# Kernel tuning notes

Hardware: AMD Instinct MI355X
Metric: run time of the kernel (lower is better)

Reference implementation:

```python
import jax, jax.numpy as jnp
import numpy as np

BN_EPS = 1e-5


def setup_inputs() -> dict:
    key = jax.random.key(0)
    ks = jax.random.split(key, 6)
    B, Adim, Bdim, E, An, Bn = 16, 512, 512, 256, 2048, 2048
    return {
        "input_A": jax.random.normal(ks[0], (B, Adim, An), jnp.float32),
        "input_B": jax.random.normal(ks[1], (B, Bdim, Bn), jnp.float32),
        "W_A": jax.random.normal(ks[2], (E, Adim), jnp.float32) * (1.0 / np.sqrt(Adim)),
        "W_B": jax.random.normal(ks[3], (E, Bdim), jnp.float32) * (1.0 / np.sqrt(Bdim)),
        "W_Bh": jax.random.normal(ks[4], (E, Bdim), jnp.float32) * (1.0 / np.sqrt(Bdim)),
        "W_out": jax.random.normal(ks[5], (Bdim, E), jnp.float32) * (1.0 / np.sqrt(E)),
        "bn_gamma": jnp.ones((Bdim,), jnp.float32),
        "bn_beta": jnp.zeros((Bdim,), jnp.float32),
    }


def reference(input_A, input_B, W_A, W_B, W_Bh, W_out, bn_gamma, bn_beta):
    # 1x1 conv == per-position linear projection over channel dim
    A = jnp.einsum("ec,bcn->ben", W_A, input_A)    # [B, E, A_n]
    Bp = jnp.einsum("ec,bcn->ben", W_B, input_B)    # [B, E, B_n]
    Bh = jnp.einsum("ec,bcn->ben", W_Bh, input_B)   # [B, E, B_n]

    norm = jnp.sqrt(jnp.float32(A.shape[1]))
    h = jnp.einsum("bea,bem->bam", A, Bp) / norm    # [B, A_n, B_n]
    att = jax.nn.softmax(h, axis=2)                 # softmax over B_n

    out = jnp.einsum("bem,bam->bea", Bh, att)       # bmm(B_h, att^T): [B, E, A_n]
    out = jnp.einsum("ce,bea->bca", W_out, out)     # [B, Bdim, A_n]

    # BatchNorm1d (training mode): per-channel stats over (batch, positions)
    mean = jnp.mean(out, axis=(0, 2), keepdims=True)
    var = jnp.mean(jnp.square(out - mean), axis=(0, 2), keepdims=True)
    out = (out - mean) * jax.lax.rsqrt(var + BN_EPS)
    out = out * bn_gamma[None, :, None] + bn_beta[None, :, None]
    return out, att
```

## Files before the change

kernel.cpp:

```cpp
#include <hip/hip_runtime.h>
#include <cstdint>
#include <cstddef>

#define BATCH 16
#define CDIM 512
#define EDIM 256
#define NDIM 2048

typedef short bf16x8 __attribute__((ext_vector_type(8)));
typedef float f32x4 __attribute__((ext_vector_type(4)));

__device__ __forceinline__ unsigned short f2bf(float f) {
  union { float f; unsigned int u; } v; v.f = f;
  unsigned int r = v.u + 0x7fffu + ((v.u >> 16) & 1u);
  return (unsigned short)(r >> 16);
}

__global__ __launch_bounds__(256) void cast_f32_bf16(const float* __restrict__ x,
                                                     unsigned short* __restrict__ y) {
  const int i = (blockIdx.x * 256 + threadIdx.x) * 4;
  float4 v = *(const float4*)&x[i];
  ushort4 o;
  o.x = f2bf(v.x); o.y = f2bf(v.y); o.z = f2bf(v.z); o.w = f2bf(v.w);
  *(ushort4*)&y[i] = o;
}

__global__ __launch_bounds__(256) void transpose_cast(const float* __restrict__ X,
                                                      unsigned short* __restrict__ Xt) {
  __shared__ float tile[32][33];
  const int b = blockIdx.z;
  const float* Xb = X + (size_t)b * CDIM * NDIM;
  unsigned short* Xtb = Xt + (size_t)b * CDIM * NDIM;
  const int n0 = blockIdx.x * 32, c0 = blockIdx.y * 32;
  const int tx = threadIdx.x & 31, ty = threadIdx.x >> 5;
#pragma unroll
  for (int i = 0; i < 4; ++i)
    tile[ty + i * 8][tx] = Xb[(size_t)(c0 + ty + i * 8) * NDIM + n0 + tx];
  __syncthreads();
  const int nl = threadIdx.x >> 3, c4 = (threadIdx.x & 7) * 4;
  ushort4 o;
  o.x = f2bf(tile[c4 + 0][nl]); o.y = f2bf(tile[c4 + 1][nl]);
  o.z = f2bf(tile[c4 + 2][nl]); o.w = f2bf(tile[c4 + 3][nl]);
  *(ushort4*)&Xtb[(size_t)(n0 + nl) * CDIM + c0 + c4] = o;
}

enum { OUT_F32 = 0, OUT_BF16 = 1, OUT_BF16T = 2 };

template <int OUTMODE, bool B_IS_F32>
__global__ __launch_bounds__(256) void gemm_nt_mfma(
    const void* __restrict__ Ap, const void* __restrict__ Bptr, void* __restrict__ Cp,
    int M, int N, int K, long sA, long sB, long sC, float scale) {
  __shared__ alignas(16) short As[128 * 72];
  __shared__ alignas(16) short Bs[128 * 72];
  const int b = blockIdx.z;
  const int m0 = blockIdx.y * 128, n0 = blockIdx.x * 128;
  const unsigned short* A = (const unsigned short*)Ap + (size_t)sA * b;
  const int tid = threadIdx.x;
  const int lane = tid & 63, wid = tid >> 6;
  const int l16 = lane & 15, q = lane >> 4;
  const int wm = (wid >> 1) * 64, wn = (wid & 1) * 64;
  const int sr = tid >> 1, sh = tid & 1;

  f32x4 acc[4][4];
#pragma unroll
  for (int i = 0; i < 4; ++i)
#pragma unroll
    for (int j = 0; j < 4; ++j) acc[i][j] = f32x4{0.f, 0.f, 0.f, 0.f};

  short* a_dst = &As[sr * 72 + sh * 32];
  short* b_dst = &Bs[sr * 72 + sh * 32];

  for (int k0 = 0; k0 < K; k0 += 64) {
    {
      const unsigned short* src = A + (size_t)(m0 + sr) * K + k0 + sh * 32;
      int4 c0 = *(const int4*)(src);
      int4 c1 = *(const int4*)(src + 8);
      int4 c2 = *(const int4*)(src + 16);
      int4 c3 = *(const int4*)(src + 24);
      *(int4*)(a_dst) = c0;
      *(int4*)(a_dst + 8) = c1;
      *(int4*)(a_dst + 16) = c2;
      *(int4*)(a_dst + 24) = c3;
    }
    if (B_IS_F32) {
      const float* src = (const float*)Bptr + (size_t)sB * b + (size_t)(n0 + sr) * K + k0 + sh * 32;
#pragma unroll
      for (int c = 0; c < 8; ++c) {
        float4 v = *(const float4*)(src + c * 4);
        ushort4 o;
        o.x = f2bf(v.x); o.y = f2bf(v.y); o.z = f2bf(v.z); o.w = f2bf(v.w);
        *(ushort4*)(b_dst + c * 4) = o;
      }
    } else {
      const unsigned short* src =
          (const unsigned short*)Bptr + (size_t)sB * b + (size_t)(n0 + sr) * K + k0 + sh * 32;
      int4 c0 = *(const int4*)(src);
      int4 c1 = *(const int4*)(src + 8);
      int4 c2 = *(const int4*)(src + 16);
      int4 c3 = *(const int4*)(src + 24);
      *(int4*)(b_dst) = c0;
      *(int4*)(b_dst + 8) = c1;
      *(int4*)(b_dst + 16) = c2;
      *(int4*)(b_dst + 24) = c3;
    }
    __syncthreads();
#pragma unroll
    for (int kk = 0; kk < 2; ++kk) {
      bf16x8 af[4], bfr[4];
#pragma unroll
      for (int t = 0; t < 4; ++t)
        af[t] = *(const bf16x8*)&As[(wm + t * 16 + l16) * 72 + kk * 32 + q * 8];
#pragma unroll
      for (int t = 0; t < 4; ++t)
        bfr[t] = *(const bf16x8*)&Bs[(wn + t * 16 + l16) * 72 + kk * 32 + q * 8];
#pragma unroll
      for (int i = 0; i < 4; ++i)
#pragma unroll
        for (int j = 0; j < 4; ++j)
          acc[i][j] = __builtin_amdgcn_mfma_f32_16x16x32_bf16(af[i], bfr[j], acc[i][j], 0, 0, 0);
    }
    __syncthreads();
  }

  const int mb = m0 + wm + q * 4, nb = n0 + wn + l16;
  if (OUTMODE == OUT_F32) {
    float* C = (float*)Cp + (size_t)sC * b;
#pragma unroll
    for (int i = 0; i < 4; ++i)
#pragma unroll
      for (int j = 0; j < 4; ++j)
#pragma unroll
        for (int r = 0; r < 4; ++r)
          C[(size_t)(mb + i * 16 + r) * N + nb + j * 16] = acc[i][j][r] * scale;
  } else if (OUTMODE == OUT_BF16) {
    unsigned short* C = (unsigned short*)Cp + (size_t)sC * b;
#pragma unroll
    for (int i = 0; i < 4; ++i)
#pragma unroll
      for (int j = 0; j < 4; ++j)
#pragma unroll
        for (int r = 0; r < 4; ++r)
          C[(size_t)(mb + i * 16 + r) * N + nb + j * 16] = f2bf(acc[i][j][r]);
  } else {
    unsigned short* C = (unsigned short*)Cp + (size_t)sC * b;
#pragma unroll
    for (int i = 0; i < 4; ++i)
#pragma unroll
      for (int j = 0; j < 4; ++j) {
        ushort4 o;
        o.x = f2bf(acc[i][j][0]); o.y = f2bf(acc[i][j][1]);
        o.z = f2bf(acc[i][j][2]); o.w = f2bf(acc[i][j][3]);
        *(ushort4*)&C[(size_t)(nb + j * 16) * M + mb + i * 16] = o;
      }
  }
}

__global__ __launch_bounds__(256) void softmax_rows(float* __restrict__ att) {
  float4* p = (float4*)(att + (size_t)blockIdx.x * NDIM);
  const int tid = threadIdx.x;
  float4 v0 = p[tid];
  float4 v1 = p[tid + 256];

  float m = fmaxf(fmaxf(fmaxf(v0.x, v0.y), fmaxf(v0.z, v0.w)),
                  fmaxf(fmaxf(v1.x, v1.y), fmaxf(v1.z, v1.w)));
#pragma unroll
  for (int off = 32; off; off >>= 1) m = fmaxf(m, __shfl_down(m, off));
  __shared__ float redm[4];
  if ((tid & 63) == 0) redm[tid >> 6] = m;
  __syncthreads();
  m = fmaxf(fmaxf(redm[0], redm[1]), fmaxf(redm[2], redm[3]));

  v0.x = __expf(v0.x - m); v0.y = __expf(v0.y - m);
  v0.z = __expf(v0.z - m); v0.w = __expf(v0.w - m);
  v1.x = __expf(v1.x - m); v1.y = __expf(v1.y - m);
  v1.z = __expf(v1.z - m); v1.w = __expf(v1.w - m);

  float s = v0.x + v0.y + v0.z + v0.w + v1.x + v1.y + v1.z + v1.w;
#pragma unroll
  for (int off = 32; off; off >>= 1) s += __shfl_down(s, off);
  __shared__ float reds[4];
  if ((tid & 63) == 0) reds[tid >> 6] = s;
  __syncthreads();
  s = reds[0] + reds[1] + reds[2] + reds[3];

  const float inv = 1.0f / s;
  v0.x *= inv; v0.y *= inv; v0.z *= inv; v0.w *= inv;
  v1.x *= inv; v1.y *= inv; v1.z *= inv; v1.w *= inv;
  p[tid] = v0;
  p[tid + 256] = v1;
}

__global__ __launch_bounds__(256) void bn_stats(const float* __restrict__ o,
                                                float* __restrict__ mean,
                                                float* __restrict__ rstd) {
  const int c = blockIdx.x;
  const int tid = threadIdx.x;
  float s = 0.f, sq = 0.f;
  for (int b = 0; b < BATCH; ++b) {
    const float4* p = (const float4*)(o + ((size_t)b * CDIM + c) * NDIM);
    float4 v = p[tid];
    float4 w = p[tid + 256];
    s += v.x + v.y + v.z + v.w + w.x + w.y + w.z + w.w;
    sq += v.x * v.x + v.y * v.y + v.z * v.z + v.w * v.w +
          w.x * w.x + w.y * w.y + w.z * w.z + w.w * w.w;
  }
#pragma unroll
  for (int off = 32; off; off >>= 1) {
    s += __shfl_down(s, off);
    sq += __shfl_down(sq, off);
  }
  __shared__ float rs[4], rq[4];
  if ((tid & 63) == 0) { rs[tid >> 6] = s; rq[tid >> 6] = sq; }
  __syncthreads();
  if (tid == 0) {
    s = rs[0] + rs[1] + rs[2] + rs[3];
    sq = rq[0] + rq[1] + rq[2] + rq[3];
    const float invn = 1.0f / (BATCH * NDIM);
    float mu = s * invn;
    float var = sq * invn - mu * mu;
    mean[c] = mu;
    rstd[c] = rsqrtf(var + 1e-5f);
  }
}

__global__ __launch_bounds__(256) void bn_norm(float* __restrict__ o,
                                               const float* __restrict__ mean,
                                               const float* __restrict__ rstd,
                                               const float* __restrict__ gamma,
                                               const float* __restrict__ beta) {
  const size_t i = (size_t)blockIdx.x * 256 + threadIdx.x;
  const int c = (int)((i >> 9) & (CDIM - 1));
  float4 v = ((float4*)o)[i];
  const float a = rstd[c] * gamma[c];
  const float d = beta[c] - mean[c] * a;
  v.x = v.x * a + d; v.y = v.y * a + d;
  v.z = v.z * a + d; v.w = v.w * a + d;
  ((float4*)o)[i] = v;
}

extern "C" void kernel_launch(void* const* d_in, const int* in_sizes, int n_in,
                              void* d_out, int out_size, void* d_ws, size_t ws_size,
                              hipStream_t stream) {
  const float* input_A = (const float*)d_in[0];
  const float* input_B = (const float*)d_in[1];
  const float* W_A   = (const float*)d_in[2];
  const float* W_B   = (const float*)d_in[3];
  const float* W_Bh  = (const float*)d_in[4];
  const float* W_out = (const float*)d_in[5];
  const float* gamma = (const float*)d_in[6];
  const float* beta  = (const float*)d_in[7];

  float* out = (float*)d_out;
  float* att = out + (size_t)BATCH * CDIM * NDIM;

  char* w = (char*)d_ws;
  unsigned short* wA  = (unsigned short*)(w + 0);
  unsigned short* wB  = (unsigned short*)(w + 262144);
  unsigned short* wBh = (unsigned short*)(w + 524288);
  unsigned short* wO  = (unsigned short*)(w + 786432);
  float* mean = (float*)(w + 1048576);
  float* rstd = (float*)(w + 1050624);
  char* base = w + 1056768;
  unsigned short* X_At = (unsigned short*)(base);
  unsigned short* X_Bt = (unsigned short*)(base + 33554432);
  unsigned short* A_t  = (unsigned short*)(base + 67108864);
  unsigned short* Bp_t = (unsigned short*)(base);
  unsigned short* Bh   = (unsigned short*)(base + 16777216);
  unsigned short* oute = (unsigned short*)(base + 67108864);

  const dim3 blk(256);

  cast_f32_bf16<<<dim3(128), blk, 0, stream>>>(W_A, wA);
  cast_f32_bf16<<<dim3(128), blk, 0, stream>>>(W_B, wB);
  cast_f32_bf16<<<dim3(128), blk, 0, stream>>>(W_Bh, wBh);
  cast_f32_bf16<<<dim3(128), blk, 0, stream>>>(W_out, wO);

  transpose_cast<<<dim3(64, 16, BATCH), blk, 0, stream>>>(input_A, X_At);
  transpose_cast<<<dim3(64, 16, BATCH), blk, 0, stream>>>(input_B, X_Bt);

  gemm_nt_mfma<OUT_BF16, false><<<dim3(2, 16, BATCH), blk, 0, stream>>>(
      X_At, wA, A_t, 2048, 256, 512, 1048576, 0, 524288, 1.f);
  gemm_nt_mfma<OUT_BF16, false><<<dim3(2, 16, BATCH), blk, 0, stream>>>(
      X_Bt, wB, Bp_t, 2048, 256, 512, 1048576, 0, 524288, 1.f);
  gemm_nt_mfma<OUT_BF16, false><<<dim3(16, 2, BATCH), blk, 0, stream>>>(
      wBh, X_Bt, Bh, 256, 2048, 512, 0, 1048576, 524288, 1.f);
  gemm_nt_mfma<OUT_F32, false><<<dim3(16, 16, BATCH), blk, 0, stream>>>(
      A_t, Bp_t, att, 2048, 2048, 256, 524288, 524288, 4194304, 0.0625f);

  softmax_rows<<<dim3(BATCH * NDIM), blk, 0, stream>>>(att);

  gemm_nt_mfma<OUT_BF16T, true><<<dim3(16, 2, BATCH), blk, 0, stream>>>(
      Bh, att, oute, 256, 2048, 2048, 524288, 4194304, 524288, 1.f);

  gemm_nt_mfma<OUT_F32, false><<<dim3(16, 4, BATCH), blk, 0, stream>>>(
      wO, oute, out, 512, 2048, 256, 0, 524288, 1048576, 1.f);

  bn_stats<<<dim3(CDIM), blk, 0, stream>>>(out, mean, rstd);
  bn_norm<<<dim3(16384), blk, 0, stream>>>(out, mean, rstd, gamma, beta);
}
```

Baseline: 768.3 us.

## Fuse attention score GEMM with row softmax in one kernel

Replaces the separate QK-style GEMM that wrote fp32 scores plus the row softmax kernel with one kernel. Each block computes a 16-row strip across all 2048 columns, keeping the scores in registers while double-buffering B tiles in LDS. It then does the max, exp and sum reductions and writes the normalized probabilities once. This removes one full write and read of the 256MB fp32 score tensor. In exchange each block does only small 16-row MFMA tiles, holds 128 accumulator registers, and stores with a strided pattern.

```diff
diff --git a/kernel.cpp b/kernel.cpp
--- a/kernel.cpp
+++ b/kernel.cpp
@@ -155,39 +155,125 @@
   }
 }
 
-__global__ __launch_bounds__(256) void softmax_rows(float* __restrict__ att) {
-  float4* p = (float4*)(att + (size_t)blockIdx.x * NDIM);
+#define BPAD 264
+
+__global__ __launch_bounds__(256, 2) void g3_softmax(
+    const unsigned short* __restrict__ At, const unsigned short* __restrict__ Bt,
+    float* __restrict__ att) {
+  __shared__ alignas(16) short As[16 * BPAD];
+  __shared__ alignas(16) short Bs[2][64 * BPAD];
+  __shared__ float redm[4][16];
+  __shared__ float reds[4][16];
+
+  const int b = blockIdx.y;
+  const int a0 = blockIdx.x * 16;
+  const unsigned short* Ab = At + (size_t)b * (NDIM * EDIM) + (size_t)a0 * EDIM;
+  const unsigned short* Bb = Bt + (size_t)b * (NDIM * EDIM);
   const int tid = threadIdx.x;
-  float4 v0 = p[tid];
-  float4 v1 = p[tid + 256];
-
-  float m = fmaxf(fmaxf(fmaxf(v0.x, v0.y), fmaxf(v0.z, v0.w)),
-                  fmaxf(fmaxf(v1.x, v1.y), fmaxf(v1.z, v1.w)));
-#pragma unroll
-  for (int off = 32; off; off >>= 1) m = fmaxf(m, __shfl_down(m, off));
-  __shared__ float redm[4];
-  if ((tid & 63) == 0) redm[tid >> 6] = m;
-  __syncthreads();
-  m = fmaxf(fmaxf(redm[0], redm[1]), fmaxf(redm[2], redm[3]));
-
-  v0.x = __expf(v0.x - m); v0.y = __expf(v0.y - m);
-  v0.z = __expf(v0.z - m); v0.w = __expf(v0.w - m);
-  v1.x = __expf(v1.x - m); v1.y = __expf(v1.y - m);
-  v1.z = __expf(v1.z - m); v1.w = __expf(v1.w - m);
-
-  float s = v0.x + v0.y + v0.z + v0.w + v1.x + v1.y + v1.z + v1.w;
-#pragma unroll
-  for (int off = 32; off; off >>= 1) s += __shfl_down(s, off);
-  __shared__ float reds[4];
-  if ((tid & 63) == 0) reds[tid >> 6] = s;
-  __syncthreads();
-  s = reds[0] + reds[1] + reds[2] + reds[3];
-
-  const float inv = 1.0f / s;
-  v0.x *= inv; v0.y *= inv; v0.z *= inv; v0.w *= inv;
-  v1.x *= inv; v1.y *= inv; v1.z *= inv; v1.w *= inv;
-  p[tid] = v0;
-  p[tid + 256] = v1;
+  const int lane = tid & 63, w = tid >> 6;
+  const int l16 = lane & 15, q = lane >> 4;
+
+  {
+    const int r = tid >> 3, c4 = (tid & 7) * 32;
+    const int4* src = (const int4*)(Ab + r * EDIM + c4);
+    int4 v0 = src[0], v1 = src[1], v2 = src[2], v3 = src[3];
+    int4* dst = (int4*)&As[r * BPAD + c4];
+    dst[0] = v0; dst[1] = v1; dst[2] = v2; dst[3] = v3;
+  }
+  __syncthreads();
+  bf16x8 af[8];
+#pragma unroll
+  for (int kk = 0; kk < 8; ++kk)
+    af[kk] = *(const bf16x8*)&As[l16 * BPAD + kk * 32 + q * 8];
+
+  const int br = tid >> 2, bc = (tid & 3) * 64;
+  const unsigned short* bsrc0 = Bb + br * EDIM + bc;
+  {
+    int4* dst = (int4*)&Bs[0][br * BPAD + bc];
+    const int4* src = (const int4*)bsrc0;
+#pragma unroll
+    for (int i = 0; i < 8; ++i) dst[i] = src[i];
+  }
+  __syncthreads();
+
+  f32x4 acc[32];
+  const int bs_off = (w * 16 + l16) * BPAD;
+#pragma unroll
+  for (int c = 0; c < 32; ++c) {
+    int4 stg[8];
+    if (c < 31) {
+      const int4* src = (const int4*)(bsrc0 + (size_t)(c + 1) * (64 * EDIM));
+#pragma unroll
+      for (int i = 0; i < 8; ++i) stg[i] = src[i];
+    }
+    const short* bp = &Bs[c & 1][bs_off];
+    f32x4 e = f32x4{0.f, 0.f, 0.f, 0.f}, o = f32x4{0.f, 0.f, 0.f, 0.f};
+#pragma unroll
+    for (int kk = 0; kk < 8; kk += 2) {
+      bf16x8 b0 = *(const bf16x8*)(bp + kk * 32 + q * 8);
+      bf16x8 b1 = *(const bf16x8*)(bp + (kk + 1) * 32 + q * 8);
+      e = __builtin_amdgcn_mfma_f32_16x16x32_bf16(af[kk], b0, e, 0, 0, 0);
+      o = __builtin_amdgcn_mfma_f32_16x16x32_bf16(af[kk + 1], b1, o, 0, 0, 0);
+    }
+    acc[c] = e + o;
+    if (c < 31) {
+      int4* dst = (int4*)&Bs[(c + 1) & 1][br * BPAD + bc];
+#pragma unroll
+      for (int i = 0; i < 8; ++i) dst[i] = stg[i];
+    }
+    __syncthreads();
+  }
+
+  float mr[4];
+#pragma unroll
+  for (int r = 0; r < 4; ++r) {
+    float m = acc[0][r];
+#pragma unroll
+    for (int c = 1; c < 32; ++c) m = fmaxf(m, acc[c][r]);
+#pragma unroll
+    for (int off = 1; off < 16; off <<= 1) m = fmaxf(m, __shfl_xor(m, off));
+    mr[r] = m;
+  }
+  if (l16 == 0) {
+#pragma unroll
+    for (int r = 0; r < 4; ++r) redm[w][q * 4 + r] = mr[r];
+  }
+  __syncthreads();
+#pragma unroll
+  for (int r = 0; r < 4; ++r) {
+    const int row = q * 4 + r;
+    mr[r] = fmaxf(fmaxf(redm[0][row], redm[1][row]),
+                  fmaxf(redm[2][row], redm[3][row]));
+  }
+  float sr[4] = {0.f, 0.f, 0.f, 0.f};
+#pragma unroll
+  for (int c = 0; c < 32; ++c) {
+#pragma unroll
+    for (int r = 0; r < 4; ++r) {
+      float p = __expf((acc[c][r] - mr[r]) * 0.0625f);
+      acc[c][r] = p;
+      sr[r] += p;
+    }
+  }
+#pragma unroll
+  for (int r = 0; r < 4; ++r)
+#pragma unroll
+    for (int off = 1; off < 16; off <<= 1) sr[r] += __shfl_xor(sr[r], off);
+  if (l16 == 0) {
+#pragma unroll
+    for (int r = 0; r < 4; ++r) reds[w][q * 4 + r] = sr[r];
+  }
+  __syncthreads();
+  float* ob = att + (size_t)b * NDIM * NDIM;
+  const int colb = w * 16 + l16;
+#pragma unroll
+  for (int r = 0; r < 4; ++r) {
+    const int row = q * 4 + r;
+    const float inv = 1.0f / (reds[0][row] + reds[1][row] + reds[2][row] + reds[3][row]);
+    float* orow = ob + (size_t)(a0 + row) * NDIM + colb;
+#pragma unroll
+    for (int c = 0; c < 32; ++c) orow[c * 64] = acc[c][r] * inv;
+  }
 }
 
 __global__ __launch_bounds__(256) void bn_stats(const float* __restrict__ o,
@@ -284,10 +370,8 @@
       X_Bt, wB, Bp_t, 2048, 256, 512, 1048576, 0, 524288, 1.f);
   gemm_nt_mfma<OUT_BF16, false><<<dim3(16, 2, BATCH), blk, 0, stream>>>(
       wBh, X_Bt, Bh, 256, 2048, 512, 0, 1048576, 524288, 1.f);
-  gemm_nt_mfma<OUT_F32, false><<<dim3(16, 16, BATCH), blk, 0, stream>>>(
-      A_t, Bp_t, att, 2048, 2048, 256, 524288, 524288, 4194304, 0.0625f);
-
-  softmax_rows<<<dim3(BATCH * NDIM), blk, 0, stream>>>(att);
+
+  g3_softmax<<<dim3(128, BATCH), blk, 0, stream>>>(A_t, Bp_t, att);
 
   gemm_nt_mfma<OUT_BF16T, true><<<dim3(16, 2, BATCH), blk, 0, stream>>>(
       Bh, att, oute, 256, 2048, 2048, 524288, 4194304, 524288, 1.f);
```

Measured after the change: 1.127 ms. 46.7% more time.

## Fuse attention score GEMM with row softmax in one kernel

Applied to the files above, without the earlier changes.

Replaces the separate QK^T GEMM (writing f32 scores) and the row-softmax kernel with a single kernel. Each 512-thread block computes 16 full rows of 2048 scores in registers with MFMA, then does the max, exp and sum reductions via shuffles and shared memory and writes normalized probabilities once. This removes one full write and a read-modify-write of the 256MB score matrix. In exchange each block reads B tiles directly from global memory with no LDS reuse, which raises L2 traffic and register pressure.

```diff
diff --git a/kernel.cpp b/kernel.cpp
--- a/kernel.cpp
+++ b/kernel.cpp
@@ -155,39 +155,143 @@
   }
 }
 
-__global__ __launch_bounds__(256) void softmax_rows(float* __restrict__ att) {
-  float4* p = (float4*)(att + (size_t)blockIdx.x * NDIM);
+__global__ __launch_bounds__(512, 2) void g3_softmax(
+    const unsigned short* __restrict__ At, const unsigned short* __restrict__ Bt,
+    float* __restrict__ att) {
+  __shared__ float redm[8][16];
+  __shared__ float reds[8][16];
+
+  const int b = blockIdx.y;
+  const int a0 = blockIdx.x * 16;
   const int tid = threadIdx.x;
-  float4 v0 = p[tid];
-  float4 v1 = p[tid + 256];
-
-  float m = fmaxf(fmaxf(fmaxf(v0.x, v0.y), fmaxf(v0.z, v0.w)),
-                  fmaxf(fmaxf(v1.x, v1.y), fmaxf(v1.z, v1.w)));
-#pragma unroll
-  for (int off = 32; off; off >>= 1) m = fmaxf(m, __shfl_down(m, off));
-  __shared__ float redm[4];
-  if ((tid & 63) == 0) redm[tid >> 6] = m;
+  const int lane = tid & 63, w = tid >> 6;
+  const int l16 = lane & 15, q = lane >> 4;
+
+  const unsigned short* Ab = At + (size_t)b * (NDIM * EDIM) + (size_t)a0 * EDIM;
+  const unsigned short* Bb = Bt + (size_t)b * (NDIM * EDIM);
+
+  const unsigned short* ap = Ab + l16 * EDIM + q * 8;
+  const bf16x8 af0 = *(const bf16x8*)(ap + 0 * 32);
+  const bf16x8 af1 = *(const bf16x8*)(ap + 1 * 32);
+  const bf16x8 af2 = *(const bf16x8*)(ap + 2 * 32);
+  const bf16x8 af3 = *(const bf16x8*)(ap + 3 * 32);
+  const bf16x8 af4 = *(const bf16x8*)(ap + 4 * 32);
+  const bf16x8 af5 = *(const bf16x8*)(ap + 5 * 32);
+  const bf16x8 af6 = *(const bf16x8*)(ap + 6 * 32);
+  const bf16x8 af7 = *(const bf16x8*)(ap + 7 * 32);
+
+  const unsigned short* bpbase = Bb + (size_t)(w * 16 + l16) * EDIM + q * 8;
+
+#define G3_MFMA __builtin_amdgcn_mfma_f32_16x16x32_bf16
+#define G3_CHUNK(C, ACC)                                                     \
+  do {                                                                       \
+    const unsigned short* bp_ = bpbase + (size_t)(C) * (128 * EDIM);         \
+    bf16x8 b0_ = *(const bf16x8*)(bp_ + 0 * 32);                             \
+    bf16x8 b1_ = *(const bf16x8*)(bp_ + 1 * 32);                             \
+    bf16x8 b2_ = *(const bf16x8*)(bp_ + 2 * 32);                             \
+    bf16x8 b3_ = *(const bf16x8*)(bp_ + 3 * 32);                             \
+    bf16x8 b4_ = *(const bf16x8*)(bp_ + 4 * 32);                             \
+    bf16x8 b5_ = *(const bf16x8*)(bp_ + 5 * 32);                             \
+    bf16x8 b6_ = *(const bf16x8*)(bp_ + 6 * 32);                             \
+    bf16x8 b7_ = *(const bf16x8*)(bp_ + 7 * 32);                             \
+    f32x4 e_ = G3_MFMA(af0, b0_, f32x4{0.f, 0.f, 0.f, 0.f}, 0, 0, 0);        \
+    f32x4 o_ = G3_MFMA(af1, b1_, f32x4{0.f, 0.f, 0.f, 0.f}, 0, 0, 0);        \
+    e_ = G3_MFMA(af2, b2_, e_, 0, 0, 0);                                     \
+    o_ = G3_MFMA(af3, b3_, o_, 0, 0, 0);                                     \
+    e_ = G3_MFMA(af4, b4_, e_, 0, 0, 0);                                     \
+    o_ = G3_MFMA(af5, b5_, o_, 0, 0, 0);                                     \
+    e_ = G3_MFMA(af6, b6_, e_, 0, 0, 0);                                     \
+    o_ = G3_MFMA(af7, b7_, o_, 0, 0, 0);                                     \
+    ACC = e_ + o_;                                                           \
+  } while (0)
+
+  f32x4 acc0, acc1, acc2, acc3, acc4, acc5, acc6, acc7;
+  f32x4 acc8, acc9, acc10, acc11, acc12, acc13, acc14, acc15;
+  G3_CHUNK(0, acc0);   G3_CHUNK(1, acc1);   G3_CHUNK(2, acc2);
+  G3_CHUNK(3, acc3);   G3_CHUNK(4, acc4);   G3_CHUNK(5, acc5);
+  G3_CHUNK(6, acc6);   G3_CHUNK(7, acc7);   G3_CHUNK(8, acc8);
+  G3_CHUNK(9, acc9);   G3_CHUNK(10, acc10); G3_CHUNK(11, acc11);
+  G3_CHUNK(12, acc12); G3_CHUNK(13, acc13); G3_CHUNK(14, acc14);
+  G3_CHUNK(15, acc15);
+
+  float mr0 = acc0[0], mr1 = acc0[1], mr2 = acc0[2], mr3 = acc0[3];
+#define G3_MAXA(ACC)                                                         \
+  do {                                                                       \
+    mr0 = fmaxf(mr0, ACC[0]); mr1 = fmaxf(mr1, ACC[1]);                      \
+    mr2 = fmaxf(mr2, ACC[2]); mr3 = fmaxf(mr3, ACC[3]);                      \
+  } while (0)
+  G3_MAXA(acc1);  G3_MAXA(acc2);  G3_MAXA(acc3);  G3_MAXA(acc4);
+  G3_MAXA(acc5);  G3_MAXA(acc6);  G3_MAXA(acc7);  G3_MAXA(acc8);
+  G3_MAXA(acc9);  G3_MAXA(acc10); G3_MAXA(acc11); G3_MAXA(acc12);
+  G3_MAXA(acc13); G3_MAXA(acc14); G3_MAXA(acc15);
+#pragma unroll
+  for (int off = 1; off < 16; off <<= 1) {
+    mr0 = fmaxf(mr0, __shfl_xor(mr0, off));
+    mr1 = fmaxf(mr1, __shfl_xor(mr1, off));
+    mr2 = fmaxf(mr2, __shfl_xor(mr2, off));
+    mr3 = fmaxf(mr3, __shfl_xor(mr3, off));
+  }
+  if (l16 == 0) {
+    redm[w][q * 4 + 0] = mr0; redm[w][q * 4 + 1] = mr1;
+    redm[w][q * 4 + 2] = mr2; redm[w][q * 4 + 3] = mr3;
+  }
   __syncthreads();
-  m = fmaxf(fmaxf(redm[0], redm[1]), fmaxf(redm[2], redm[3]));
-
-  v0.x = __expf(v0.x - m); v0.y = __expf(v0.y - m);
-  v0.z = __expf(v0.z - m); v0.w = __expf(v0.w - m);
-  v1.x = __expf(v1.x - m); v1.y = __expf(v1.y - m);
-  v1.z = __expf(v1.z - m); v1.w = __expf(v1.w - m);
-
-  float s = v0.x + v0.y + v0.z + v0.w + v1.x + v1.y + v1.z + v1.w;
-#pragma unroll
-  for (int off = 32; off; off >>= 1) s += __shfl_down(s, off);
-  __shared__ float reds[4];
-  if ((tid & 63) == 0) reds[tid >> 6] = s;
+#define G3_RED8(ARR, R)                                                       \
+  fmaxf(fmaxf(fmaxf(ARR[0][R], ARR[1][R]), fmaxf(ARR[2][R], ARR[3][R])),      \
+        fmaxf(fmaxf(ARR[4][R], ARR[5][R]), fmaxf(ARR[6][R], ARR[7][R])))
+  mr0 = G3_RED8(redm, q * 4 + 0);
+  mr1 = G3_RED8(redm, q * 4 + 1);
+  mr2 = G3_RED8(redm, q * 4 + 2);
+  mr3 = G3_RED8(redm, q * 4 + 3);
+
+  float sr0 = 0.f, sr1 = 0.f, sr2 = 0.f, sr3 = 0.f;
+#define G3_EXPA(ACC)                                                         \
+  do {                                                                       \
+    ACC[0] = __expf((ACC[0] - mr0) * 0.0625f); sr0 += ACC[0];                \
+    ACC[1] = __expf((ACC[1] - mr1) * 0.0625f); sr1 += ACC[1];                \
+    ACC[2] = __expf((ACC[2] - mr2) * 0.0625f); sr2 += ACC[2];                \
+    ACC[3] = __expf((ACC[3] - mr3) * 0.0625f); sr3 += ACC[3];                \
+  } while (0)
+  G3_EXPA(acc0);  G3_EXPA(acc1);  G3_EXPA(acc2);  G3_EXPA(acc3);
+  G3_EXPA(acc4);  G3_EXPA(acc5);  G3_EXPA(acc6);  G3_EXPA(acc7);
+  G3_EXPA(acc8);  G3_EXPA(acc9);  G3_EXPA(acc10); G3_EXPA(acc11);
+  G3_EXPA(acc12); G3_EXPA(acc13); G3_EXPA(acc14); G3_EXPA(acc15);
+#pragma unroll
+  for (int off = 1; off < 16; off <<= 1) {
+    sr0 += __shfl_xor(sr0, off);
+    sr1 += __shfl_xor(sr1, off);
+    sr2 += __shfl_xor(sr2, off);
+    sr3 += __shfl_xor(sr3, off);
+  }
+  if (l16 == 0) {
+    reds[w][q * 4 + 0] = sr0; reds[w][q * 4 + 1] = sr1;
+    reds[w][q * 4 + 2] = sr2; reds[w][q * 4 + 3] = sr3;
+  }
   __syncthreads();
-  s = reds[0] + reds[1] + reds[2] + reds[3];
-
-  const float inv = 1.0f / s;
-  v0.x *= inv; v0.y *= inv; v0.z *= inv; v0.w *= inv;
-  v1.x *= inv; v1.y *= inv; v1.z *= inv; v1.w *= inv;
-  p[tid] = v0;
-  p[tid + 256] = v1;
+#define G3_SUM8(ARR, R)                                                      \
+  (((ARR[0][R] + ARR[1][R]) + (ARR[2][R] + ARR[3][R])) +                     \
+   ((ARR[4][R] + ARR[5][R]) + (ARR[6][R] + ARR[7][R])))
+  const float inv0 = 1.0f / G3_SUM8(reds, q * 4 + 0);
+  const float inv1 = 1.0f / G3_SUM8(reds, q * 4 + 1);
+  const float inv2 = 1.0f / G3_SUM8(reds, q * 4 + 2);
+  const float inv3 = 1.0f / G3_SUM8(reds, q * 4 + 3);
+
+  float* ob = att + (size_t)b * NDIM * NDIM + (size_t)a0 * NDIM + w * 16 + l16;
+  float* orow0 = ob + (size_t)(q * 4 + 0) * NDIM;
+  float* orow1 = ob + (size_t)(q * 4 + 1) * NDIM;
+  float* orow2 = ob + (size_t)(q * 4 + 2) * NDIM;
+  float* orow3 = ob + (size_t)(q * 4 + 3) * NDIM;
+#define G3_WRA(C, ACC)                                                       \
+  do {                                                                       \
+    orow0[(C) * 128] = ACC[0] * inv0;                                        \
+    orow1[(C) * 128] = ACC[1] * inv1;                                        \
+    orow2[(C) * 128] = ACC[2] * inv2;                                        \
+    orow3[(C) * 128] = ACC[3] * inv3;                                        \
+  } while (0)
+  G3_WRA(0, acc0);   G3_WRA(1, acc1);   G3_WRA(2, acc2);   G3_WRA(3, acc3);
+  G3_WRA(4, acc4);   G3_WRA(5, acc5);   G3_WRA(6, acc6);   G3_WRA(7, acc7);
+  G3_WRA(8, acc8);   G3_WRA(9, acc9);   G3_WRA(10, acc10); G3_WRA(11, acc11);
+  G3_WRA(12, acc12); G3_WRA(13, acc13); G3_WRA(14, acc14); G3_WRA(15, acc15);
 }
 
 __global__ __launch_bounds__(256) void bn_stats(const float* __restrict__ o,
@@ -284,10 +388,8 @@
       X_Bt, wB, Bp_t, 2048, 256, 512, 1048576, 0, 524288, 1.f);
   gemm_nt_mfma<OUT_BF16, false><<<dim3(16, 2, BATCH), blk, 0, stream>>>(
       wBh, X_Bt, Bh, 256, 2048, 512, 0, 1048576, 524288, 1.f);
-  gemm_nt_mfma<OUT_F32, false><<<dim3(16, 16, BATCH), blk, 0, stream>>>(
-      A_t, Bp_t, att, 2048, 2048, 256, 524288, 524288, 4194304, 0.0625f);
-
-  softmax_rows<<<dim3(BATCH * NDIM), blk, 0, stream>>>(att);
+
+  g3_softmax<<<dim3(128, BATCH), dim3(512), 0, stream>>>(A_t, Bp_t, att);
 
   gemm_nt_mfma<OUT_BF16T, true><<<dim3(16, 2, BATCH), blk, 0, stream>>>(
       Bh, att, oute, 256, 2048, 2048, 524288, 4194304, 524288, 1.f);
```

Result: slower. 885.1 us (+15.2%).
